# Kernel tuning notes

Measured on AMD Instinct MI355X. Metric: run time of the kernel, lower is better.

## Reference

```python
import jax, jax.numpy as jnp
import numpy as np

B = 128        # graphs in batch
GW = 30        # grid width (nodes per graph = GW*GW)
IW = 90        # image width = 3*GW for k=7,s=3,p=2 conv transpose
C_IN = 32
HID = [64, 64, 32]
R = 8          # num relations
NB = 4         # num bases
N = B * GW * GW          # 115200 nodes
E = N * 8                # 921600 edges
NEG_SLOPE = 0.01         # F.leaky_relu default


def setup_inputs() -> dict:
    key = jax.random.key(0)
    ks = jax.random.split(key, 24)
    inp = {
        "features": jax.random.normal(ks[0], (N, C_IN), jnp.float32),
        "src": jax.random.randint(ks[1], (E,), 0, N),
        "dst": jax.random.randint(ks[2], (E,), 0, N),
        "etypes": jax.random.randint(ks[3], (E,), 0, R),
        "norm": jax.random.uniform(ks[4], (E,), jnp.float32),
    }
    dims = [C_IN] + HID
    for l in range(3):
        din, dout = dims[l], dims[l + 1]
        s = 1.0 / np.sqrt(din)
        inp[f"bases{l}"] = jax.random.normal(ks[5 + 4 * l], (NB, din, dout), jnp.float32) * s
        inp[f"comp{l}"] = jax.random.normal(ks[6 + 4 * l], (R, NB), jnp.float32) * (1.0 / np.sqrt(NB))
        inp[f"loop{l}"] = jax.random.normal(ks[7 + 4 * l], (din, dout), jnp.float32) * s
        inp[f"bias{l}"] = jnp.zeros((dout,), jnp.float32)
    inp["conv_w"] = jax.random.normal(ks[20], (HID[-1], 1, 7, 7), jnp.float32) * 0.05  # torch ConvT layout (Cin,Cout,kH,kW)
    inp["conv_b"] = jnp.zeros((1,), jnp.float32)
    return inp


def _rel_graph_conv(h, bases, comp, loop_w, bias, src, dst, etypes, norm, act):
    # basis decomposition: W_r = sum_b comp[r,b] * bases[b]   -> (R, in, out)
    W = jnp.einsum("rb,bio->rio", comp, bases)
    # project every node by every relation weight, then gather per edge
    proj = jnp.einsum("ni,rio->nro", h, W)          # (N, R, out)
    msg = proj[src, etypes] * norm[:, None]          # (E, out)
    agg = jax.ops.segment_sum(msg, dst, num_segments=h.shape[0])
    out = agg + h @ loop_w + bias                    # self-loop + bias (DGL defaults)
    return act(out)


def _conv_transpose(x, w_torch, b, stride, pad):
    # torch ConvTranspose2d(w: (Cin,Cout,kH,kW)) == dilated conv with flipped kernel
    k = w_torch.shape[-1]
    w = jnp.flip(w_torch, (2, 3)).transpose(1, 0, 2, 3)  # -> OIHW
    p = k - 1 - pad
    y = jax.lax.conv_general_dilated(
        x, w, window_strides=(1, 1), padding=[(p, p), (p, p)],
        lhs_dilation=(stride, stride),
        dimension_numbers=("NCHW", "OIHW", "NCHW"))
    return y + b[None, :, None, None]


def reference(features, src, dst, etypes, norm,
              bases0, comp0, loop0, bias0,
              bases1, comp1, loop1, bias1,
              bases2, comp2, loop2, bias2,
              conv_w, conv_b):
    leaky = lambda x: jnp.where(x >= 0, x, NEG_SLOPE * x)
    h = _rel_graph_conv(features, bases0, comp0, loop0, bias0, src, dst, etypes, norm, leaky)
    h = _rel_graph_conv(h, bases1, comp1, loop1, bias1, src, dst, etypes, norm, leaky)
    logits = _rel_graph_conv(h, bases2, comp2, loop2, bias2, src, dst, etypes, norm, jax.nn.sigmoid)
    # every graph has exactly GW*GW nodes -> vectorized decode (replaces per-graph loop)
    x = logits.reshape(B, GW, GW, HID[-1]).transpose(0, 3, 1, 2)  # (B, C, GW, GW)
    y = jax.nn.sigmoid(_conv_transpose(x, conv_w, conv_b, stride=3, pad=2))  # (B,1,IW,IW)
    return y.reshape(B, IW, IW)
```

## Files before the change

### kernel.cpp

```cpp
#include <hip/hip_runtime.h>
#include <hip/hip_bf16.h>

#define B_GR   128
#define GWID   30
#define IWID   90
#define C_IN   32
#define R_REL  8
#define NBAS   4
#define N_NODES (B_GR*GWID*GWID)
#define E_EDGES (N_NODES*8)
#define NEG_SLOPE 0.01f

#define SCAN_BLOCKS (N_NODES/256)

typedef __attribute__((ext_vector_type(8))) __bf16 bf16x8;
typedef __attribute__((ext_vector_type(4))) float f32x4;

__global__ void k_bases_t(const float* __restrict__ bases, __bf16* __restrict__ Bt,
                          int din, int dout) {
    int idx = blockIdx.x*256 + threadIdx.x;
    int tot = NBAS*din*dout;
    if (idx >= tot) return;
    int b = idx/(dout*din), rem = idx%(dout*din);
    int c = rem/din, k = rem%din;
    Bt[idx] = (__bf16)bases[((size_t)b*din + k)*dout + c];
}
__global__ void k_loop_t(const float* __restrict__ loopw, __bf16* __restrict__ loopt,
                         int din, int dout) {
    int idx = blockIdx.x*256 + threadIdx.x;
    if (idx >= din*dout) return;
    int c = idx/din, k = idx%din;
    loopt[idx] = (__bf16)loopw[(size_t)k*dout + c];
}

__global__ void k_deg(const int* __restrict__ dst, int* __restrict__ deg) {
    int e = blockIdx.x*256 + threadIdx.x;
    if (e < E_EDGES) atomicAdd(&deg[dst[e]], 1);
}
__global__ __launch_bounds__(256) void k_scan1(const int* __restrict__ deg,
                                               int* __restrict__ rowptr,
                                               int* __restrict__ bsum) {
    __shared__ int s[256], s2[256];
    const int tid = threadIdx.x, gid = blockIdx.x*256 + tid;
    int v = deg[gid];
    s[tid] = v;
    __syncthreads();
    int* cur = s; int* nxt = s2;
    for (int d = 1; d < 256; d <<= 1) {
        int val = cur[tid];
        if (tid >= d) val += cur[tid - d];
        nxt[tid] = val;
        __syncthreads();
        int* t = cur; cur = nxt; nxt = t;
    }
    rowptr[gid] = cur[tid] - v;
    if (tid == 255) bsum[blockIdx.x] = cur[255];
}
__global__ __launch_bounds__(512) void k_scan2(int* __restrict__ bsum, int* __restrict__ rowptr) {
    __shared__ int s[512], s2[512];
    const int tid = threadIdx.x;
    int v = (tid < SCAN_BLOCKS) ? bsum[tid] : 0;
    s[tid] = v;
    __syncthreads();
    int* cur = s; int* nxt = s2;
    for (int d = 1; d < 512; d <<= 1) {
        int val = cur[tid];
        if (tid >= d) val += cur[tid - d];
        nxt[tid] = val;
        __syncthreads();
        int* t = cur; cur = nxt; nxt = t;
    }
    if (tid < SCAN_BLOCKS) bsum[tid] = cur[tid] - v;
    if (tid == 0) rowptr[N_NODES] = E_EDGES;
}
__global__ void k_scan3(int* __restrict__ rowptr, const int* __restrict__ bsum,
                        int* __restrict__ cursor) {
    int gid = blockIdx.x*256 + threadIdx.x;
    int v = rowptr[gid] + bsum[blockIdx.x];
    rowptr[gid] = v;
    cursor[gid] = v;
}
__global__ void k_scatter_pack(const int* __restrict__ src, const int* __restrict__ dst,
                               const int* __restrict__ et, const float* __restrict__ norm,
                               int* __restrict__ cursor, int* __restrict__ ppack,
                               float* __restrict__ pnorm) {
    int e = blockIdx.x*256 + threadIdx.x;
    if (e < E_EDGES) {
        int pos = atomicAdd(&cursor[dst[e]], 1);
        ppack[pos] = src[e] | (et[e] << 24);
        pnorm[pos] = norm[e];
    }
}

template<int DIN, int DOUT, int ACT, int IN_F32, int OUT_F32>
__global__ __launch_bounds__(256) void k_fusedb(
        const void* __restrict__ hin, const __bf16* __restrict__ Bt,
        const __bf16* __restrict__ loopt, const float* __restrict__ bias,
        const float* __restrict__ comp, const int* __restrict__ rowptr,
        const int* __restrict__ ppack, const float* __restrict__ pnorm,
        void* __restrict__ hout) {
    constexpr int KS = DIN/32;
    constexpr int NF = DOUT/16;
    const int tid = threadIdx.x;
    const int w = tid >> 6, l = tid & 63;
    const int m = l & 15, g = l >> 4;
    const int nb = blockIdx.x*64 + w*16;
    const int node = nb + m;

    f32x4 acc[NF];
    #pragma unroll
    for (int nf = 0; nf < NF; ++nf) acc[nf] = (f32x4){0.f,0.f,0.f,0.f};

    float ka[NBAS][KS][8];
    #pragma unroll
    for (int b = 0; b < NBAS; ++b)
        #pragma unroll
        for (int ks = 0; ks < KS; ++ks)
            #pragma unroll
            for (int c = 0; c < 8; ++c) ka[b][ks][c] = 0.f;

    const int jb = rowptr[node], je = rowptr[node+1];
    for (int j = jb; j < je; ++j) {
        const int pk = ppack[j];
        const float nm = pnorm[j];
        const int p = pk & 0xFFFFFF;
        const int et = pk >> 24;
        const float4 cw = *(const float4*)(comp + et*NBAS);
        const float w0 = nm*cw.x, w1 = nm*cw.y, w2 = nm*cw.z, w3 = nm*cw.w;
        float hv[KS][8];
        if (IN_F32) {
            const float* hp = (const float*)hin + (size_t)p*DIN + g*8;
            #pragma unroll
            for (int ks = 0; ks < KS; ++ks) {
                float4 v0 = *(const float4*)(hp + ks*32);
                float4 v1 = *(const float4*)(hp + ks*32 + 4);
                hv[ks][0]=v0.x; hv[ks][1]=v0.y; hv[ks][2]=v0.z; hv[ks][3]=v0.w;
                hv[ks][4]=v1.x; hv[ks][5]=v1.y; hv[ks][6]=v1.z; hv[ks][7]=v1.w;
            }
        } else {
            const __bf16* hp = (const __bf16*)hin + (size_t)p*DIN + g*8;
            #pragma unroll
            for (int ks = 0; ks < KS; ++ks) {
                bf16x8 v = *(const bf16x8*)(hp + ks*32);
                #pragma unroll
                for (int c = 0; c < 8; ++c) hv[ks][c] = (float)v[c];
            }
        }
        #pragma unroll
        for (int ks = 0; ks < KS; ++ks) {
            #pragma unroll
            for (int c = 0; c < 8; ++c) {
                ka[0][ks][c] += w0*hv[ks][c];
                ka[1][ks][c] += w1*hv[ks][c];
                ka[2][ks][c] += w2*hv[ks][c];
                ka[3][ks][c] += w3*hv[ks][c];
            }
        }
    }

    #pragma unroll
    for (int b = 0; b < NBAS; ++b) {
        #pragma unroll
        for (int ks = 0; ks < KS; ++ks) {
            bf16x8 fa;
            #pragma unroll
            for (int c = 0; c < 8; ++c) fa[c] = (__bf16)ka[b][ks][c];
            #pragma unroll
            for (int nf = 0; nf < NF; ++nf) {
                bf16x8 fb = *(const bf16x8*)(Bt + ((size_t)b*DOUT + nf*16 + m)*DIN
                                             + ks*32 + g*8);
                acc[nf] = __builtin_amdgcn_mfma_f32_16x16x32_bf16(fa, fb, acc[nf], 0, 0, 0);
            }
        }
    }

    #pragma unroll
    for (int ks = 0; ks < KS; ++ks) {
        bf16x8 fa;
        if (IN_F32) {
            const float* hp = (const float*)hin + (size_t)node*DIN + ks*32 + g*8;
            float4 v0 = *(const float4*)hp;
            float4 v1 = *(const float4*)(hp + 4);
            fa[0]=(__bf16)v0.x; fa[1]=(__bf16)v0.y; fa[2]=(__bf16)v0.z; fa[3]=(__bf16)v0.w;
            fa[4]=(__bf16)v1.x; fa[5]=(__bf16)v1.y; fa[6]=(__bf16)v1.z; fa[7]=(__bf16)v1.w;
        } else {
            fa = *(const bf16x8*)((const __bf16*)hin + (size_t)node*DIN + ks*32 + g*8);
        }
        #pragma unroll
        for (int nf = 0; nf < NF; ++nf) {
            bf16x8 fb = *(const bf16x8*)(loopt + (size_t)(nf*16 + m)*DIN + ks*32 + g*8);
            acc[nf] = __builtin_amdgcn_mfma_f32_16x16x32_bf16(fa, fb, acc[nf], 0, 0, 0);
        }
    }

    #pragma unroll
    for (int nf = 0; nf < NF; ++nf) {
        const int col = nf*16 + m;
        const float bv = bias[col];
        #pragma unroll
        for (int ri = 0; ri < 4; ++ri) {
            const int orow = nb + g*4 + ri;
            float v = acc[nf][ri] + bv;
            if (ACT == 0) v = (v >= 0.f) ? v : NEG_SLOPE*v;
            else          v = 1.f/(1.f + __expf(-v));
            if (OUT_F32) ((float*)hout)[(size_t)orow*DOUT + col] = v;
            else         ((__bf16*)hout)[(size_t)orow*DOUT + col] = (__bf16)v;
        }
    }
}

__global__ __launch_bounds__(256) void k_convt_f32(const float* __restrict__ logits,
        const float* __restrict__ w, const float* __restrict__ cb, float* __restrict__ out) {
    __shared__ float s_w[49*32];
    const int tid = threadIdx.x;
    for (int idx = tid; idx < 49*32; idx += 256) {
        int tap = idx/32, c = idx%32;
        s_w[tap*32 + c] = w[c*49 + tap];
    }
    __syncthreads();
    int gidx = blockIdx.x*256 + tid;
    if (gidx >= B_GR*IWID*IWID) return;
    int b = gidx/(IWID*IWID);
    int rem = gidx%(IWID*IWID);
    int oy = rem/IWID, ox = rem%IWID;

    const int py = (oy+2)%3, qy = (oy+2)/3;
    const int px = (ox+2)%3, qx = (ox+2)/3;

    float acc = cb[0];
    #pragma unroll
    for (int sy = 0; sy < 3; ++sy) {
        const int ky = py + 3*sy;
        const int iy = qy - sy;
        if (ky > 6 || iy < 0 || iy >= GWID) continue;
        #pragma unroll
        for (int sx = 0; sx < 3; ++sx) {
            const int kx = px + 3*sx;
            const int ix = qx - sx;
            if (kx > 6 || ix < 0 || ix >= GWID) continue;
            const float4* xp = (const float4*)&logits[(((size_t)b*GWID + iy)*GWID + ix)*32];
            const float4* wp = (const float4*)&s_w[(ky*7 + kx)*32];
            #pragma unroll
            for (int c4 = 0; c4 < 8; ++c4) {
                float4 xv = xp[c4], wv = wp[c4];
                acc += xv.x*wv.x + xv.y*wv.y + xv.z*wv.z + xv.w*wv.w;
            }
        }
    }
    out[gidx] = 1.f/(1.f + __expf(-acc));
}

extern "C" void kernel_launch(void* const* d_in, const int* in_sizes, int n_in,
                              void* d_out, int out_size, void* d_ws, size_t ws_size,
                              hipStream_t stream) {
    const float* features = (const float*)d_in[0];
    const int*   src      = (const int*)  d_in[1];
    const int*   dst      = (const int*)  d_in[2];
    const int*   etypes   = (const int*)  d_in[3];
    const float* norm     = (const float*)d_in[4];
    const float* bases0 = (const float*)d_in[5];
    const float* comp0  = (const float*)d_in[6];
    const float* loop0  = (const float*)d_in[7];
    const float* bias0  = (const float*)d_in[8];
    const float* bases1 = (const float*)d_in[9];
    const float* comp1  = (const float*)d_in[10];
    const float* loop1  = (const float*)d_in[11];
    const float* bias1  = (const float*)d_in[12];
    const float* bases2 = (const float*)d_in[13];
    const float* comp2  = (const float*)d_in[14];
    const float* loop2  = (const float*)d_in[15];
    const float* bias2  = (const float*)d_in[16];
    const float* conv_w = (const float*)d_in[17];
    const float* conv_b = (const float*)d_in[18];
    float* out = (float*)d_out;

    const int ebl = (E_EDGES + 255)/256;
    float* ws = (float*)d_ws;
    auto pad4 = [](size_t v){ return (v + 3) & ~(size_t)3; };

    size_t off = 0;
    __bf16* Bt0   = (__bf16*)(ws + off); off += (size_t)NBAS*32*64/2;
    __bf16* Bt1   = (__bf16*)(ws + off); off += (size_t)NBAS*64*64/2;
    __bf16* Bt2   = (__bf16*)(ws + off); off += (size_t)NBAS*64*32/2;
    __bf16* lt0   = (__bf16*)(ws + off); off += (size_t)64*32/2;
    __bf16* lt1   = (__bf16*)(ws + off); off += (size_t)64*64/2;
    __bf16* lt2   = (__bf16*)(ws + off); off += (size_t)32*64/2;
    __bf16* h1    = (__bf16*)(ws + off); off += (size_t)N_NODES*64/2;
    __bf16* h2    = (__bf16*)(ws + off); off += (size_t)N_NODES*64/2;
    float*  lg    = (float*)(ws + off);  off += (size_t)N_NODES*32;
    int* rowptr   = (int*)(ws + off); off += pad4((size_t)N_NODES + 4);
    int* deg      = (int*)(ws + off); off += (size_t)N_NODES;
    int* bsum     = (int*)(ws + off); off += 512;
    int* ppack    = (int*)(ws + off); off += (size_t)E_EDGES;
    float* pnorm  = ws + off;          off += (size_t)E_EDGES;

    k_bases_t<<<(NBAS*32*64 + 255)/256, 256, 0, stream>>>(bases0, Bt0, 32, 64);
    k_bases_t<<<(NBAS*64*64 + 255)/256, 256, 0, stream>>>(bases1, Bt1, 64, 64);
    k_bases_t<<<(NBAS*64*32 + 255)/256, 256, 0, stream>>>(bases2, Bt2, 64, 32);
    k_loop_t<<<(32*64 + 255)/256, 256, 0, stream>>>(loop0, lt0, 32, 64);
    k_loop_t<<<(64*64 + 255)/256, 256, 0, stream>>>(loop1, lt1, 64, 64);
    k_loop_t<<<(64*32 + 255)/256, 256, 0, stream>>>(loop2, lt2, 64, 32);

    hipMemsetAsync(deg, 0, (size_t)N_NODES*sizeof(int), stream);
    k_deg  <<<ebl, 256, 0, stream>>>(dst, deg);
    k_scan1<<<SCAN_BLOCKS, 256, 0, stream>>>(deg, rowptr, bsum);
    k_scan2<<<1, 512, 0, stream>>>(bsum, rowptr);
    k_scan3<<<SCAN_BLOCKS, 256, 0, stream>>>(rowptr, bsum, deg);
    k_scatter_pack<<<ebl, 256, 0, stream>>>(src, dst, etypes, norm, deg, ppack, pnorm);

    const int NROWT = N_NODES/64;

    k_fusedb<32,64,0,1,0><<<NROWT, 256, 0, stream>>>(features, Bt0, lt0, bias0, comp0,
                                                     rowptr, ppack, pnorm, h1);
    k_fusedb<64,64,0,0,0><<<NROWT, 256, 0, stream>>>(h1, Bt1, lt1, bias1, comp1,
                                                     rowptr, ppack, pnorm, h2);
    k_fusedb<64,32,1,0,1><<<NROWT, 256, 0, stream>>>(h2, Bt2, lt2, bias2, comp2,
                                                     rowptr, ppack, pnorm, lg);

    k_convt_f32<<<(B_GR*IWID*IWID + 255)/256, 256, 0, stream>>>(lg, conv_w, conv_b, out);
}
```

Before: 344.7 us.

## Interleave edge metadata and split gather by k-slice to cut register pressure

Packs each edge's src/type and norm into one int2 array so each edge needs a single 8-byte load instead of two separate loads. The fused layer kernel now loops over the edge list once per 32-wide input slice, accumulating only a [4][8] basis accumulator before issuing MFMAs for that slice. This cuts live registers, and the launch bound now requests 4 blocks per CU to raise occupancy. In exchange, edge metadata and comp coefficients are re-read once per slice for the 64-wide layers, and the row gathers become narrower per pass.

```diff
diff --git a/kernel.cpp b/kernel.cpp
--- a/kernel.cpp
+++ b/kernel.cpp
@@ -82,23 +82,23 @@
 }
 __global__ void k_scatter_pack(const int* __restrict__ src, const int* __restrict__ dst,
                                const int* __restrict__ et, const float* __restrict__ norm,
-                               int* __restrict__ cursor, int* __restrict__ ppack,
-                               float* __restrict__ pnorm) {
+                               int* __restrict__ cursor, int2* __restrict__ pmeta) {
     int e = blockIdx.x*256 + threadIdx.x;
     if (e < E_EDGES) {
         int pos = atomicAdd(&cursor[dst[e]], 1);
-        ppack[pos] = src[e] | (et[e] << 24);
-        pnorm[pos] = norm[e];
+        int2 m;
+        m.x = src[e] | (et[e] << 24);
+        m.y = __float_as_int(norm[e]);
+        pmeta[pos] = m;
     }
 }
 
 template<int DIN, int DOUT, int ACT, int IN_F32, int OUT_F32>
-__global__ __launch_bounds__(256) void k_fusedb(
+__global__ __launch_bounds__(256, 4) void k_fusedb(
         const void* __restrict__ hin, const __bf16* __restrict__ Bt,
         const __bf16* __restrict__ loopt, const float* __restrict__ bias,
         const float* __restrict__ comp, const int* __restrict__ rowptr,
-        const int* __restrict__ ppack, const float* __restrict__ pnorm,
-        void* __restrict__ hout) {
+        const int2* __restrict__ pmeta, void* __restrict__ hout) {
     constexpr int KS = DIN/32;
     constexpr int NF = DOUT/16;
     const int tid = threadIdx.x;
@@ -111,60 +111,49 @@
     #pragma unroll
     for (int nf = 0; nf < NF; ++nf) acc[nf] = (f32x4){0.f,0.f,0.f,0.f};
 
-    float ka[NBAS][KS][8];
-    #pragma unroll
-    for (int b = 0; b < NBAS; ++b)
-        #pragma unroll
-        for (int ks = 0; ks < KS; ++ks)
-            #pragma unroll
-            for (int c = 0; c < 8; ++c) ka[b][ks][c] = 0.f;
-
     const int jb = rowptr[node], je = rowptr[node+1];
-    for (int j = jb; j < je; ++j) {
-        const int pk = ppack[j];
-        const float nm = pnorm[j];
-        const int p = pk & 0xFFFFFF;
-        const int et = pk >> 24;
-        const float4 cw = *(const float4*)(comp + et*NBAS);
-        const float w0 = nm*cw.x, w1 = nm*cw.y, w2 = nm*cw.z, w3 = nm*cw.w;
-        float hv[KS][8];
-        if (IN_F32) {
-            const float* hp = (const float*)hin + (size_t)p*DIN + g*8;
-            #pragma unroll
-            for (int ks = 0; ks < KS; ++ks) {
-                float4 v0 = *(const float4*)(hp + ks*32);
-                float4 v1 = *(const float4*)(hp + ks*32 + 4);
-                hv[ks][0]=v0.x; hv[ks][1]=v0.y; hv[ks][2]=v0.z; hv[ks][3]=v0.w;
-                hv[ks][4]=v1.x; hv[ks][5]=v1.y; hv[ks][6]=v1.z; hv[ks][7]=v1.w;
+
+    #pragma unroll
+    for (int ks = 0; ks < KS; ++ks) {
+        float ka[NBAS][8];
+        #pragma unroll
+        for (int b = 0; b < NBAS; ++b)
+            #pragma unroll
+            for (int c = 0; c < 8; ++c) ka[b][c] = 0.f;
+
+        for (int j = jb; j < je; ++j) {
+            const int2 mt = pmeta[j];
+            const int p = mt.x & 0xFFFFFF;
+            const int et = ((unsigned)mt.x) >> 24;
+            const float nm = __int_as_float(mt.y);
+            const float4 cw = *(const float4*)(comp + et*NBAS);
+            const float w0 = nm*cw.x, w1 = nm*cw.y, w2 = nm*cw.z, w3 = nm*cw.w;
+            float hv[8];
+            if (IN_F32) {
+                const float* hp = (const float*)hin + (size_t)p*DIN + ks*32 + g*8;
+                float4 v0 = *(const float4*)hp;
+                float4 v1 = *(const float4*)(hp + 4);
+                hv[0]=v0.x; hv[1]=v0.y; hv[2]=v0.z; hv[3]=v0.w;
+                hv[4]=v1.x; hv[5]=v1.y; hv[6]=v1.z; hv[7]=v1.w;
+            } else {
+                bf16x8 v = *(const bf16x8*)((const __bf16*)hin + (size_t)p*DIN + ks*32 + g*8);
+                #pragma unroll
+                for (int c = 0; c < 8; ++c) hv[c] = (float)v[c];
             }
-        } else {
-            const __bf16* hp = (const __bf16*)hin + (size_t)p*DIN + g*8;
-            #pragma unroll
-            for (int ks = 0; ks < KS; ++ks) {
-                bf16x8 v = *(const bf16x8*)(hp + ks*32);
-                #pragma unroll
-                for (int c = 0; c < 8; ++c) hv[ks][c] = (float)v[c];
+            #pragma unroll
+            for (int c = 0; c < 8; ++c) {
+                ka[0][c] += w0*hv[c];
+                ka[1][c] += w1*hv[c];
+                ka[2][c] += w2*hv[c];
+                ka[3][c] += w3*hv[c];
             }
         }
-        #pragma unroll
-        for (int ks = 0; ks < KS; ++ks) {
-            #pragma unroll
-            for (int c = 0; c < 8; ++c) {
-                ka[0][ks][c] += w0*hv[ks][c];
-                ka[1][ks][c] += w1*hv[ks][c];
-                ka[2][ks][c] += w2*hv[ks][c];
-                ka[3][ks][c] += w3*hv[ks][c];
-            }
-        }
-    }
-
-    #pragma unroll
-    for (int b = 0; b < NBAS; ++b) {
-        #pragma unroll
-        for (int ks = 0; ks < KS; ++ks) {
+
+        #pragma unroll
+        for (int b = 0; b < NBAS; ++b) {
             bf16x8 fa;
             #pragma unroll
-            for (int c = 0; c < 8; ++c) fa[c] = (__bf16)ka[b][ks][c];
+            for (int c = 0; c < 8; ++c) fa[c] = (__bf16)ka[b][c];
             #pragma unroll
             for (int nf = 0; nf < NF; ++nf) {
                 bf16x8 fb = *(const bf16x8*)(Bt + ((size_t)b*DOUT + nf*16 + m)*DIN
@@ -291,8 +280,7 @@
     int* rowptr   = (int*)(ws + off); off += pad4((size_t)N_NODES + 4);
     int* deg      = (int*)(ws + off); off += (size_t)N_NODES;
     int* bsum     = (int*)(ws + off); off += 512;
-    int* ppack    = (int*)(ws + off); off += (size_t)E_EDGES;
-    float* pnorm  = ws + off;          off += (size_t)E_EDGES;
+    int2* pmeta   = (int2*)(ws + off); off += (size_t)E_EDGES*2;
 
     k_bases_t<<<(NBAS*32*64 + 255)/256, 256, 0, stream>>>(bases0, Bt0, 32, 64);
     k_bases_t<<<(NBAS*64*64 + 255)/256, 256, 0, stream>>>(bases1, Bt1, 64, 64);
@@ -306,16 +294,16 @@
     k_scan1<<<SCAN_BLOCKS, 256, 0, stream>>>(deg, rowptr, bsum);
     k_scan2<<<1, 512, 0, stream>>>(bsum, rowptr);
     k_scan3<<<SCAN_BLOCKS, 256, 0, stream>>>(rowptr, bsum, deg);
-    k_scatter_pack<<<ebl, 256, 0, stream>>>(src, dst, etypes, norm, deg, ppack, pnorm);
+    k_scatter_pack<<<ebl, 256, 0, stream>>>(src, dst, etypes, norm, deg, pmeta);
 
     const int NROWT = N_NODES/64;
 
     k_fusedb<32,64,0,1,0><<<NROWT, 256, 0, stream>>>(features, Bt0, lt0, bias0, comp0,
-                                                     rowptr, ppack, pnorm, h1);
+                                                     rowptr, pmeta, h1);
     k_fusedb<64,64,0,0,0><<<NROWT, 256, 0, stream>>>(h1, Bt1, lt1, bias1, comp1,
-                                                     rowptr, ppack, pnorm, h2);
+                                                     rowptr, pmeta, h2);
     k_fusedb<64,32,1,0,1><<<NROWT, 256, 0, stream>>>(h2, Bt2, lt2, bias2, comp2,
-                                                     rowptr, ppack, pnorm, lg);
+                                                     rowptr, pmeta, lg);
 
     k_convt_f32<<<(B_GR*IWID*IWID + 255)/256, 256, 0, stream>>>(lg, conv_w, conv_b, out);
 }
```

Result: slower. 374.8 us (+8.7%).
